# Performance work log

Hardware: AMD Instinct MI355X
Metric: run time of the kernel (lower is better)

The kernel has to match this reference:

```python
import jax, jax.numpy as jnp
import numpy as np

B, L, D, N = 2, 2048, 1024, 16
H = D // N  # head dim 64
MASK_FILL = -100000000.0  # torch code uses -1e8 for non-fp16


def sinusoidal_pos(seq_len, dim):
    # interleaved (sin, cos) table, shape (seq_len, dim); identical per head
    inv_freq = 1.0 / (10000.0 ** (jnp.arange(0, dim, 2, dtype=jnp.float32) / dim))
    ang = jnp.arange(seq_len, dtype=jnp.float32)[:, None] * inv_freq[None, :]
    return jnp.stack([jnp.sin(ang), jnp.cos(ang)], axis=-1).reshape(seq_len, dim)


def apply_rope(x, pos_emb):
    # x: (b, n, l, h); pos_emb: (l, h) interleaved sin/cos
    cos = jnp.repeat(pos_emb[..., 1::2], 2, axis=-1)  # (l, h)
    sin = jnp.repeat(pos_emb[..., ::2], 2, axis=-1)
    x2 = jnp.stack([-x[..., 1::2], x[..., ::2]], axis=-1).reshape(x.shape)
    return x * cos + x2 * sin


def setup_inputs() -> dict:
    key = jax.random.key(0)
    ks = jax.random.split(key, 12)
    inp = {
        "q": jax.random.normal(ks[0], (B, L, D), dtype=jnp.float32),
        "k": jax.random.normal(ks[1], (B, L, D), dtype=jnp.float32),
        "v": jax.random.normal(ks[2], (B, L, D), dtype=jnp.float32),
        "mask": jax.random.bernoulli(ks[3], 0.3, (B, L)),  # True = masked
    }
    s = 0.02
    for i, name in enumerate(["q", "k", "v", "o"]):
        inp[f"W{name}"] = jax.random.normal(ks[4 + i], (D, D), dtype=jnp.float32) * s
        inp[f"b{name}"] = jax.random.normal(ks[8 + i], (D,), dtype=jnp.float32) * s
    return inp


def reference(q, k, v, mask, Wq, bq, Wk, bk, Wv, bv, Wo, bo):
    # projections (torch Linear: x @ W^T + b) and head split -> (b, n, l, h)
    def split_heads(x):
        return x.reshape(B, L, N, H).transpose(0, 2, 1, 3)

    qw = split_heads(q @ Wq.T + bq)
    kw = split_heads(k @ Wk.T + bk)
    vw = split_heads(v @ Wv.T + bv)

    pos = sinusoidal_pos(L, H)
    qw = apply_rope(qw, pos)
    kw = apply_rope(kw, pos)

    # NOTE: original scales by sqrt(hidden_dim), not sqrt(head_dim)
    scores = jnp.einsum("bnlh,bnph->bnlp", qw, kw) / np.sqrt(D).astype(np.float32)
    scores = jnp.where(mask[:, None, None, :], MASK_FILL, scores)
    attn = jax.nn.softmax(scores, axis=-1)  # dropout is identity in eval

    out = jnp.einsum("bnlp,bnph->bnlh", attn, vw)  # (b, n, l, h)
    out = out.transpose(0, 2, 1, 3).reshape(B, L, D)
    return out @ Wo.T + bo
```

## Files before the change

### kernel.cpp

```cpp
#include <hip/hip_runtime.h>
#include <stdint.h>

#define L_SEQ 2048
#define DMODEL 1024
#define NHEAD 16
#define HDIM 64
#define BATCH 2
#define KVBLK 32
#define KHALF (L_SEQ / 2)
#define NKT (KHALF / KVBLK)

typedef __attribute__((ext_vector_type(8))) short bf16x8;
typedef __attribute__((ext_vector_type(4))) float f32x4;

#define MFMA(a, b, c) __builtin_amdgcn_mfma_f32_16x16x32_bf16((a), (b), (c), 0, 0, 0)

#if __has_builtin(__builtin_amdgcn_exp2f)
#define EXP2(x) __builtin_amdgcn_exp2f(x)
#else
#define EXP2(x) exp2f(x)
#endif

#if __has_builtin(__builtin_amdgcn_wave_barrier)
#define WAVE_FENCE() __builtin_amdgcn_wave_barrier()
#else
#define WAVE_FENCE() __syncthreads()
#endif

#define QSCALE 0.04508422f
#define MASKBIAS -100.0f

__device__ __forceinline__ unsigned short f2bf(float f) {
    return (unsigned short)((__float_as_uint(f) + 0x8000u) >> 16);
}
__device__ __forceinline__ float bf2f(unsigned short h) {
    return __uint_as_float(((unsigned int)h) << 16);
}
__device__ __forceinline__ unsigned int pkbf(float a, float b) {
    return __builtin_amdgcn_perm(__float_as_uint(b) + 0x8000u,
                                 __float_as_uint(a) + 0x8000u, 0x07060302u);
}
__device__ __forceinline__ void gl2lds16(const unsigned short* g, unsigned short* l) {
    __builtin_amdgcn_global_load_lds(
        (const __attribute__((address_space(1))) void*)g,
        (__attribute__((address_space(3))) void*)l, 16, 0, 0);
}

__global__ void prep_kernel(
    const float* __restrict__ q, const float* __restrict__ k, const float* __restrict__ v,
    const float* __restrict__ wq, const float* __restrict__ wk, const float* __restrict__ wv,
    const float* __restrict__ Wo, const int* __restrict__ mask,
    unsigned short* __restrict__ xb, unsigned short* __restrict__ wb,
    unsigned short* __restrict__ whi, unsigned short* __restrict__ wlo,
    float2* __restrict__ ropetab, float* __restrict__ fbias)
{
    const int y = blockIdx.y, x = blockIdx.x, tid = threadIdx.x;
    if (y < 6) {
        const float* src = (y == 0) ? q : (y == 1) ? k : (y == 2) ? v
                         : (y == 3) ? wq : (y == 4) ? wk : wv;
        unsigned short* dst = (y < 3) ? xb + (size_t)y * 4194304
                                      : wb + (size_t)(y - 3) * 1048576;
        const int n = (y < 3) ? 4194304 : 1048576;
        const int i = (x * 256 + tid) * 8;
        if (i >= n) return;
        const float4 a = *(const float4*)(src + i);
        const float4 b = *(const float4*)(src + i + 4);
        uint4 u;
        u.x = pkbf(a.x, a.y); u.y = pkbf(a.z, a.w);
        u.z = pkbf(b.x, b.y); u.w = pkbf(b.z, b.w);
        *(uint4*)(dst + i) = u;
    } else if (y == 6) {
        const int i = (x * 256 + tid) * 4;
        if (i >= DMODEL * DMODEL) return;
        const float4 vv = *(const float4*)(Wo + i);
        const float f[4] = {vv.x, vv.y, vv.z, vv.w};
        union { unsigned short s[4]; uint2 u; } h, l;
#pragma unroll
        for (int r = 0; r < 4; ++r) {
            h.s[r] = f2bf(f[r]);
            l.s[r] = f2bf(f[r] - bf2f(h.s[r]));
        }
        *(uint2*)&whi[i] = h.u;
        *(uint2*)&wlo[i] = l.u;
    } else {
        if (x < 512) {
            const int idx = x * 256 + tid;
            const int l = idx >> 6, h = idx & 63;
            const float invf = powf(10000.0f, -(float)(h & 62) * (1.0f / 64.0f));
            float sn, cs;
            sincosf((float)l * invf, &sn, &cs);
            ropetab[idx] = make_float2(cs, sn);
        } else if (x < 528) {
            const int idx = (x - 512) * 256 + tid;
            fbias[idx] = (mask[idx] != 0) ? MASKBIAS : 0.0f;
        }
    }
}

__global__ __launch_bounds__(256) void qkv_kernel(
    const unsigned short* __restrict__ Xb, const unsigned short* __restrict__ Wb,
    const float* __restrict__ bq, const float* __restrict__ bk, const float* __restrict__ bv,
    const float2* __restrict__ ropetab,
    unsigned short* __restrict__ Qd, unsigned short* __restrict__ Kd,
    unsigned short* __restrict__ Vd)
{
    const int id = blockIdx.x;
    const int bx = id / 96, rem = id % 96;
    const int z = rem >> 5, by = rem & 31;

    const unsigned short* X = Xb + (size_t)z * (BATCH * L_SEQ * DMODEL);
    const unsigned short* W = Wb + (size_t)z * (DMODEL * DMODEL);
    const float* bias = (z == 0) ? bq : (z == 1) ? bk : bv;

    __shared__ __align__(16) unsigned short As[128 * 64];
    __shared__ __align__(16) unsigned short Bs[128 * 64];

    const int tid  = threadIdx.x;
    const int wave = tid >> 6, lane = tid & 63;
    const int ml = lane & 15, kq = lane >> 4;
    const int m0 = by * 128, n0 = bx * 128;
    const int wm = (wave & 1) * 64, wn = (wave >> 1) * 64;

    f32x4 acc[4][4];
#pragma unroll
    for (int i = 0; i < 4; ++i)
#pragma unroll
        for (int j = 0; j < 4; ++j) acc[i][j] = (f32x4){0.f, 0.f, 0.f, 0.f};

    const int prow = wave * 32 + (lane >> 3);
    const int pch  = (lane & 7) ^ ((lane >> 3) & 7);
    const unsigned short* gA = X + (size_t)(m0 + prow) * DMODEL + pch * 8;
    const unsigned short* gB = W + (size_t)(n0 + prow) * DMODEL + pch * 8;
    unsigned short* lA = As + wave * 2048;
    unsigned short* lB = Bs + wave * 2048;

    for (int kc = 0; kc < DMODEL; kc += 64) {
#pragma unroll
        for (int qq = 0; qq < 4; ++qq) {
            gl2lds16(gA + kc + (size_t)qq * 8 * DMODEL, lA + qq * 512);
            gl2lds16(gB + kc + (size_t)qq * 8 * DMODEL, lB + qq * 512);
        }
        __syncthreads();

        bf16x8 af[2][4], bfv[2][4];
#pragma unroll
        for (int ks = 0; ks < 2; ++ks)
#pragma unroll
            for (int i = 0; i < 4; ++i) {
                const int Ra = wm + i * 16 + ml;
                af[ks][i] = *(const bf16x8*)&As[Ra * 64 + (((ks * 4 + kq) ^ (Ra & 7)) << 3)];
                const int Rb = wn + i * 16 + ml;
                bfv[ks][i] = *(const bf16x8*)&Bs[Rb * 64 + (((ks * 4 + kq) ^ (Rb & 7)) << 3)];
            }
#pragma unroll
        for (int ks = 0; ks < 2; ++ks)
#pragma unroll
            for (int i = 0; i < 4; ++i)
#pragma unroll
                for (int j = 0; j < 4; ++j)
                    acc[i][j] = MFMA(af[ks][i], bfv[ks][j], acc[i][j]);
        __syncthreads();
    }

    if (z < 2) {
        unsigned short* dst = (z == 0) ? Qd : Kd;
        const float osc = (z == 0) ? QSCALE : 1.0f;
#pragma unroll
        for (int jt = 0; jt < 4; ++jt) {
            const int col = n0 + wn + jt * 16 + ml;
            const float bv = bias[col];
            const int nh = col >> 6, hh = col & 63;
            const int odd = hh & 1;
#pragma unroll
            for (int it = 0; it < 4; ++it) {
#pragma unroll
                for (int r = 0; r < 4; ++r) {
                    const int row = m0 + wm + it * 16 + kq * 4 + r;
                    const int bb = row >> 11, ll = row & 2047;
                    const float v = acc[it][jt][r] + bv;
                    const float partner = __shfl_xor(v, 1);
                    const float2 cs = ropetab[ll * 64 + hh];
                    const float res = odd ? fmaf(v, cs.x, partner * cs.y)
                                          : fmaf(v, cs.x, -partner * cs.y);
                    dst[(((size_t)(bb * NHEAD + nh) * L_SEQ + ll) << 6) + hh] = f2bf(res * osc);
                }
            }
        }
    } else {
#pragma unroll
        for (int jt = 0; jt < 4; ++jt) {
            const int col = n0 + wn + jt * 16 + ml;
            const float bv = bias[col];
            const int nh = col >> 6, hh = col & 63;
#pragma unroll
            for (int it = 0; it < 4; ++it) {
                const int rb = m0 + wm + it * 16 + kq * 4;
                const int bb = rb >> 11, ll = rb & 2047;
                uint2 pk;
                pk.x = pkbf(acc[it][jt][0] + bv, acc[it][jt][1] + bv);
                pk.y = pkbf(acc[it][jt][2] + bv, acc[it][jt][3] + bv);
                *(uint2*)&Vd[(((size_t)bb * NHEAD + nh) * HDIM + hh) * L_SEQ + ll] = pk;
            }
        }
    }
}

__global__ __launch_bounds__(512, 4) void attn_kernel(
    const unsigned short* __restrict__ Qr, const unsigned short* __restrict__ Kr,
    const unsigned short* __restrict__ Vt, const float* __restrict__ fbias,
    unsigned short* __restrict__ AOhi, unsigned short* __restrict__ AOlo)
{
    __shared__ __align__(16) unsigned short lds[24832];

    const int tid  = threadIdx.x;
    const int w    = tid >> 6, lane = tid & 63;
    const int kh   = w >> 2, qg = w & 3;
    const int ml = lane & 15, kq = lane >> 4;

    const int id = blockIdx.x;
    const int xcd = id & 7, slot = id >> 3;
    const int bh = xcd * 4 + (slot & 3);
    const int qb = slot >> 2;
    const int b = bh >> 4, nh = bh & 15;
    const int q0 = qb * 128;
    const int wq = qg * 32;
    const int koff = kh * KHALF;

    const unsigned short* Qp = Qr + (size_t)bh * L_SEQ * HDIM;
    const unsigned short* Kp = Kr + (size_t)bh * L_SEQ * HDIM;
    const unsigned short* Vp = Vt + (size_t)bh * HDIM * L_SEQ;

    bf16x8 qf[2][2];
#pragma unroll
    for (int qt = 0; qt < 2; ++qt)
#pragma unroll
        for (int c = 0; c < 2; ++c)
            qf[qt][c] = *(const bf16x8*)(Qp + (size_t)(q0 + wq + qt * 16 + ml) * HDIM + c * 32 + kq * 8);

    float li[2] = {0.f, 0.f};
    f32x4 o[2][4];
#pragma unroll
    for (int qt = 0; qt < 2; ++qt)
#pragma unroll
        for (int ht = 0; ht < 4; ++ht) o[qt][ht] = (f32x4){0.f, 0.f, 0.f, 0.f};

    unsigned short* Pw = lds + 16384 + w * 1024;

    const int srow8 = lane >> 3;
    const int sch   = (lane & 7) ^ srow8;
    const unsigned short* gK = Kp + (size_t)(koff + qg * 8 + srow8) * HDIM + sch * 8;
    const int vrow = lane >> 2;
    const int vch  = (lane & 3) ^ (vrow & 3);
    const unsigned short* gV = Vp + (size_t)(qg * 16 + vrow) * L_SEQ + koff + vch * 8;

#define STAGE(kt, bf)                                                           \
    do {                                                                        \
        gl2lds16(gK + (size_t)(kt) * KVBLK * HDIM,                              \
                 lds + ((bf) * 2 + kh) * 2048 + qg * 512);                      \
        gl2lds16(gV + (kt) * KVBLK,                                             \
                 lds + 8192 + ((bf) * 2 + kh) * 2048 + qg * 512);               \
    } while (0)

    const float* fbp = fbias + (size_t)b * L_SEQ + koff + kq * 4;
    f32x4 bcur[2], bnext[2];
#pragma unroll
    for (int nt = 0; nt < 2; ++nt) bcur[nt] = *(const f32x4*)(fbp + nt * 16);

    STAGE(0, 0);

    for (int kt = 0; kt < NKT; ++kt) {
        const int buf = kt & 1;
        __syncthreads();
        if (kt + 1 < NKT) {
            STAGE(kt + 1, buf ^ 1);
#pragma unroll
            for (int nt = 0; nt < 2; ++nt)
                bnext[nt] = *(const f32x4*)(fbp + (kt + 1) * KVBLK + nt * 16);
        }

        const unsigned short* Kb = lds + (buf * 2 + kh) * 2048;
        const unsigned short* Vb = lds + 8192 + (buf * 2 + kh) * 2048;

        f32x4 st[2][2];
#pragma unroll
        for (int nt = 0; nt < 2; ++nt) {
            const int R = nt * 16 + ml;
            const bf16x8 kf0 = *(const bf16x8*)&Kb[R * 64 + ((kq ^ (R & 7)) << 3)];
            const bf16x8 kf1 = *(const bf16x8*)&Kb[R * 64 + (((4 + kq) ^ (R & 7)) << 3)];
#pragma unroll
            for (int qt = 0; qt < 2; ++qt) {
                f32x4 c = MFMA(kf0, qf[qt][0], bcur[nt]);
                c = MFMA(kf1, qf[qt][1], c);
                st[qt][nt] = c;
            }
        }

#pragma unroll
        for (int qt = 0; qt < 2; ++qt) {
#pragma unroll
            for (int nt = 0; nt < 2; ++nt) {
                float p[4];
#pragma unroll
                for (int r = 0; r < 4; ++r) {
                    p[r] = EXP2(st[qt][nt][r]);
                    li[qt] += p[r];
                }
                uint2 pk;
                pk.x = pkbf(p[0], p[1]);
                pk.y = pkbf(p[2], p[3]);
                const int row = qt * 16 + ml;
                const int cg = (nt * 2 + (kq >> 1)) ^ (row & 3);
                *(uint2*)&Pw[row * 32 + (cg << 3) + (kq & 1) * 4] = pk;
            }
        }
        WAVE_FENCE();

        bf16x8 pf[2];
#pragma unroll
        for (int qt = 0; qt < 2; ++qt) {
            const int row = qt * 16 + ml;
            pf[qt] = *(const bf16x8*)&Pw[row * 32 + ((kq ^ (row & 3)) << 3)];
        }
#pragma unroll
        for (int ht = 0; ht < 4; ++ht) {
            const int R = ht * 16 + ml;
            const bf16x8 vf = *(const bf16x8*)&Vb[R * 32 + ((kq ^ (R & 3)) << 3)];
#pragma unroll
            for (int qt = 0; qt < 2; ++qt)
                o[qt][ht] = MFMA(vf, pf[qt], o[qt][ht]);
        }
        WAVE_FENCE();

#pragma unroll
        for (int nt = 0; nt < 2; ++nt) bcur[nt] = bnext[nt];
    }
#undef STAGE

#pragma unroll
    for (int qt = 0; qt < 2; ++qt) {
        li[qt] += __shfl_xor(li[qt], 16);
        li[qt] += __shfl_xor(li[qt], 32);
    }

    float* osc = (float*)lds;
    float* lis = (float*)(lds + 24576);
    __syncthreads();
    if (kh == 1) {
#pragma unroll
        for (int qt = 0; qt < 2; ++qt)
#pragma unroll
            for (int ht = 0; ht < 4; ++ht)
                *(f32x4*)(osc + qg * 2048 + (qt * 4 + ht) * 256 + lane * 4) = o[qt][ht];
        if (kq == 0) {
            lis[qg * 32 + ml]      = li[0];
            lis[qg * 32 + 16 + ml] = li[1];
        }
    }
    __syncthreads();
    if (kh == 1) return;

#pragma unroll
    for (int qt = 0; qt < 2; ++qt) {
#pragma unroll
        for (int ht = 0; ht < 4; ++ht)
            o[qt][ht] += *(const f32x4*)(osc + qg * 2048 + (qt * 4 + ht) * 256 + lane * 4);
        li[qt] += lis[qg * 32 + qt * 16 + ml];
    }
    const float inv[2] = {1.f / li[0], 1.f / li[1]};

    unsigned short* Pe = lds + 16384 + qg * 2048;
    const int qr = lane >> 2, quarter = lane & 3;
    const int rc0 = (quarter * 2) ^ (qr & 7), rc1 = (quarter * 2 + 1) ^ (qr & 7);

#pragma unroll
    for (int qt = 0; qt < 2; ++qt)
#pragma unroll
        for (int ht = 0; ht < 4; ++ht) {
            uint2 pk;
            pk.x = pkbf(o[qt][ht][0] * inv[qt], o[qt][ht][1] * inv[qt]);
            pk.y = pkbf(o[qt][ht][2] * inv[qt], o[qt][ht][3] * inv[qt]);
            const int row = qt * 16 + ml;
            const int ck = ht * 2 + (kq >> 1);
            *(uint2*)&Pe[row * 64 + ((ck ^ (ml & 7)) << 3) + (kq & 1) * 4] = pk;
        }
    WAVE_FENCE();
#pragma unroll
    for (int qt = 0; qt < 2; ++qt) {
        const size_t gbase = ((size_t)b * L_SEQ + q0 + wq + qt * 16 + qr) * DMODEL
                             + nh * 64 + quarter * 16;
        const uint4 d0 = *(const uint4*)&Pe[(qt * 16 + qr) * 64 + (rc0 << 3)];
        const uint4 d1 = *(const uint4*)&Pe[(qt * 16 + qr) * 64 + (rc1 << 3)];
        *(uint4*)&AOhi[gbase]     = d0;
        *(uint4*)&AOhi[gbase + 8] = d1;
    }
    WAVE_FENCE();
#pragma unroll
    for (int qt = 0; qt < 2; ++qt)
#pragma unroll
        for (int ht = 0; ht < 4; ++ht) {
            float lo[4];
#pragma unroll
            for (int r = 0; r < 4; ++r) {
                const float v = o[qt][ht][r] * inv[qt];
                const float hf = __uint_as_float((__float_as_uint(v) + 0x8000u) & 0xffff0000u);
                lo[r] = v - hf;
            }
            uint2 pk;
            pk.x = pkbf(lo[0], lo[1]);
            pk.y = pkbf(lo[2], lo[3]);
            const int row = qt * 16 + ml;
            const int ck = ht * 2 + (kq >> 1);
            *(uint2*)&Pe[row * 64 + ((ck ^ (ml & 7)) << 3) + (kq & 1) * 4] = pk;
        }
    WAVE_FENCE();
#pragma unroll
    for (int qt = 0; qt < 2; ++qt) {
        const size_t gbase = ((size_t)b * L_SEQ + q0 + wq + qt * 16 + qr) * DMODEL
                             + nh * 64 + quarter * 16;
        const uint4 d0 = *(const uint4*)&Pe[(qt * 16 + qr) * 64 + (rc0 << 3)];
        const uint4 d1 = *(const uint4*)&Pe[(qt * 16 + qr) * 64 + (rc1 << 3)];
        *(uint4*)&AOlo[gbase]     = d0;
        *(uint4*)&AOlo[gbase + 8] = d1;
    }
}

__global__ __launch_bounds__(256) void oproj_kernel(
    const unsigned short* __restrict__ Ahi_g, const unsigned short* __restrict__ Alo_g,
    const unsigned short* __restrict__ Whi_g, const unsigned short* __restrict__ Wlo_g,
    const float* __restrict__ bias, float* __restrict__ out)
{
    const int id = blockIdx.x;
    const int bxn = id >> 5, by = id & 31;

    __shared__ __align__(16) unsigned short Ah[128 * 32], Al[128 * 32];
    __shared__ __align__(16) unsigned short Bh[64 * 32],  Bl[64 * 32];

    const int tid  = threadIdx.x;
    const int wave = tid >> 6, lane = tid & 63;
    const int ml = lane & 15, kq = lane >> 4;
    const int m0 = by * 128, n0 = bxn * 64;
    const int wm = (wave & 1) * 64, wn = (wave >> 1) * 32;

    f32x4 acc[4][2];
#pragma unroll
    for (int i = 0; i < 4; ++i)
#pragma unroll
        for (int j = 0; j < 2; ++j) acc[i][j] = (f32x4){0.f, 0.f, 0.f, 0.f};

    const int rl  = lane >> 2;
    const int pch = (lane & 3) ^ ((lane >> 3) & 3);
    const int prowA = wave * 32 + rl;
    const int prowB = wave * 16 + rl;
    const unsigned short* gAh = Ahi_g + (size_t)(m0 + prowA) * DMODEL + pch * 8;
    const unsigned short* gAl = Alo_g + (size_t)(m0 + prowA) * DMODEL + pch * 8;
    const unsigned short* gBh = Whi_g + (size_t)(n0 + prowB) * DMODEL + pch * 8;
    const unsigned short* gBl = Wlo_g + (size_t)(n0 + prowB) * DMODEL + pch * 8;
    unsigned short* lAh = Ah + wave * 1024;
    unsigned short* lAl = Al + wave * 1024;
    unsigned short* lBh = Bh + wave * 512;
    unsigned short* lBl = Bl + wave * 512;

    for (int kc = 0; kc < DMODEL; kc += 32) {
#pragma unroll
        for (int qq = 0; qq < 2; ++qq) {
            const size_t go = kc + (size_t)qq * 16 * DMODEL;
            gl2lds16(gAh + go, lAh + qq * 512);
            gl2lds16(gAl + go, lAl + qq * 512);
        }
        gl2lds16(gBh + kc, lBh);
        gl2lds16(gBl + kc, lBl);
        __syncthreads();

        bf16x8 ah[4], al[4], bh_[2], bl_[2];
#pragma unroll
        for (int i = 0; i < 4; ++i) {
            const int Ra = wm + i * 16 + ml;
            const int sa = Ra * 32 + ((kq ^ ((Ra >> 1) & 3)) << 3);
            ah[i] = *(const bf16x8*)&Ah[sa];
            al[i] = *(const bf16x8*)&Al[sa];
        }
#pragma unroll
        for (int j = 0; j < 2; ++j) {
            const int Rb = wn + j * 16 + ml;
            const int sb = Rb * 32 + ((kq ^ ((Rb >> 1) & 3)) << 3);
            bh_[j] = *(const bf16x8*)&Bh[sb];
            bl_[j] = *(const bf16x8*)&Bl[sb];
        }
#pragma unroll
        for (int i = 0; i < 4; ++i)
#pragma unroll
            for (int j = 0; j < 2; ++j) {
                acc[i][j] = MFMA(ah[i], bh_[j], acc[i][j]);
                acc[i][j] = MFMA(al[i], bh_[j], acc[i][j]);
                acc[i][j] = MFMA(ah[i], bl_[j], acc[i][j]);
            }
        __syncthreads();
    }

#pragma unroll
    for (int jt = 0; jt < 2; ++jt) {
        const int col = n0 + wn + jt * 16 + ml;
        const float bv = bias[col];
#pragma unroll
        for (int it = 0; it < 4; ++it)
#pragma unroll
            for (int r = 0; r < 4; ++r) {
                const int row = m0 + wm + it * 16 + kq * 4 + r;
                out[(size_t)row * DMODEL + col] = acc[it][jt][r] + bv;
            }
    }
}

extern "C" void kernel_launch(void* const* d_in, const int* in_sizes, int n_in,
                              void* d_out, int out_size, void* d_ws, size_t ws_size,
                              hipStream_t stream)
{
    (void)in_sizes; (void)n_in; (void)out_size; (void)ws_size;
    const float* q    = (const float*)d_in[0];
    const float* k    = (const float*)d_in[1];
    const float* v    = (const float*)d_in[2];
    const int*   mask = (const int*)d_in[3];
    const float* Wq   = (const float*)d_in[4];
    const float* bq   = (const float*)d_in[5];
    const float* Wk   = (const float*)d_in[6];
    const float* bk   = (const float*)d_in[7];
    const float* Wv   = (const float*)d_in[8];
    const float* bv   = (const float*)d_in[9];
    const float* Wo   = (const float*)d_in[10];
    const float* bo   = (const float*)d_in[11];
    float* out = (float*)d_out;

    const size_t HE = (size_t)BATCH * NHEAD * L_SEQ * HDIM;
    const size_t DD = (size_t)DMODEL * DMODEL;
    unsigned short* Xb   = (unsigned short*)d_ws;
    unsigned short* Wb   = Xb + 3 * HE;
    unsigned short* Qr   = Wb + 3 * DD;
    unsigned short* Kr   = Qr + HE;
    unsigned short* Vt   = Kr + HE;
    unsigned short* Whi  = Vt + HE;
    unsigned short* Wlo  = Whi + DD;
    float* fbias = (float*)(Wlo + DD);
    float2* ropetab = (float2*)(fbias + (size_t)BATCH * L_SEQ);
    unsigned short* AOhi = Xb;
    unsigned short* AOlo = Xb + HE;

    prep_kernel<<<dim3(2048, 8), dim3(256), 0, stream>>>(
        q, k, v, Wq, Wk, Wv, Wo, mask, Xb, Wb, Whi, Wlo, ropetab, fbias);

    qkv_kernel<<<dim3(768), dim3(256), 0, stream>>>(Xb, Wb, bq, bk, bv, ropetab, Qr, Kr, Vt);

    attn_kernel<<<dim3(512), dim3(512), 0, stream>>>(Qr, Kr, Vt, fbias, AOhi, AOlo);

    oproj_kernel<<<dim3(512), dim3(256), 0, stream>>>(AOhi, AOlo, Whi, Wlo, bo, out);
}
```

Baseline: 246.5 us.

## Halve attention block to 4 waves, each handling 64 query rows

The attention kernel now runs 256 threads (4 waves) instead of 512. Each wave processes 64 query rows instead of 32, so every K/V fragment read from LDS feeds twice as many MFMAs, and staging, swizzle and epilogue offsets are adjusted to match. This cuts LDS traffic and barrier participants per unit of work, but raises register pressure (larger o/st/qf arrays) and halves per-block parallelism, which may lower occupancy or latency hiding.

```diff
diff --git a/kernel.cpp b/kernel.cpp
--- a/kernel.cpp
+++ b/kernel.cpp
@@ -205,7 +205,7 @@
     }
 }
 
-__global__ __launch_bounds__(512, 4) void attn_kernel(
+__global__ __launch_bounds__(256) void attn_kernel(
     const unsigned short* __restrict__ Qr, const unsigned short* __restrict__ Kr,
     const unsigned short* __restrict__ Vt, const float* __restrict__ fbias,
     unsigned short* __restrict__ AOhi, unsigned short* __restrict__ AOlo)
@@ -214,8 +214,9 @@
 
     const int tid  = threadIdx.x;
     const int w    = tid >> 6, lane = tid & 63;
-    const int kh   = w >> 2, qg = w & 3;
+    const int kh   = w >> 1, qg = w & 1;
     const int ml = lane & 15, kq = lane >> 4;
+    const int swz = (ml >> 1) & 3;
 
     const int id = blockIdx.x;
     const int xcd = id & 7, slot = id >> 3;
@@ -223,42 +224,44 @@
     const int qb = slot >> 2;
     const int b = bh >> 4, nh = bh & 15;
     const int q0 = qb * 128;
-    const int wq = qg * 32;
+    const int wq = qg * 64;
     const int koff = kh * KHALF;
 
     const unsigned short* Qp = Qr + (size_t)bh * L_SEQ * HDIM;
     const unsigned short* Kp = Kr + (size_t)bh * L_SEQ * HDIM;
     const unsigned short* Vp = Vt + (size_t)bh * HDIM * L_SEQ;
 
-    bf16x8 qf[2][2];
-#pragma unroll
-    for (int qt = 0; qt < 2; ++qt)
+    bf16x8 qf[4][2];
+#pragma unroll
+    for (int qt = 0; qt < 4; ++qt)
 #pragma unroll
         for (int c = 0; c < 2; ++c)
             qf[qt][c] = *(const bf16x8*)(Qp + (size_t)(q0 + wq + qt * 16 + ml) * HDIM + c * 32 + kq * 8);
 
-    float li[2] = {0.f, 0.f};
-    f32x4 o[2][4];
-#pragma unroll
-    for (int qt = 0; qt < 2; ++qt)
+    float li[4] = {0.f, 0.f, 0.f, 0.f};
+    f32x4 o[4][4];
+#pragma unroll
+    for (int qt = 0; qt < 4; ++qt)
 #pragma unroll
         for (int ht = 0; ht < 4; ++ht) o[qt][ht] = (f32x4){0.f, 0.f, 0.f, 0.f};
 
-    unsigned short* Pw = lds + 16384 + w * 1024;
+    unsigned short* Pw = lds + 16384 + w * 2048;
 
     const int srow8 = lane >> 3;
     const int sch   = (lane & 7) ^ srow8;
-    const unsigned short* gK = Kp + (size_t)(koff + qg * 8 + srow8) * HDIM + sch * 8;
+    const unsigned short* gK = Kp + (size_t)(koff + qg * 16 + srow8) * HDIM + sch * 8;
     const int vrow = lane >> 2;
-    const int vch  = (lane & 3) ^ (vrow & 3);
-    const unsigned short* gV = Vp + (size_t)(qg * 16 + vrow) * L_SEQ + koff + vch * 8;
+    const int vch  = (lane & 3) ^ ((vrow >> 1) & 3);
+    const unsigned short* gV = Vp + (size_t)(qg * 32 + vrow) * L_SEQ + koff + vch * 8;
 
 #define STAGE(kt, bf)                                                           \
     do {                                                                        \
-        gl2lds16(gK + (size_t)(kt) * KVBLK * HDIM,                              \
-                 lds + ((bf) * 2 + kh) * 2048 + qg * 512);                      \
-        gl2lds16(gV + (kt) * KVBLK,                                             \
-                 lds + 8192 + ((bf) * 2 + kh) * 2048 + qg * 512);               \
+        unsigned short* kb = lds + ((bf) * 2 + kh) * 2048 + qg * 1024;          \
+        unsigned short* vb = lds + 8192 + ((bf) * 2 + kh) * 2048 + qg * 1024;   \
+        gl2lds16(gK + (size_t)(kt) * KVBLK * HDIM, kb);                         \
+        gl2lds16(gK + (size_t)((kt) * KVBLK + 8) * HDIM, kb + 512);             \
+        gl2lds16(gV + (kt) * KVBLK, vb);                                        \
+        gl2lds16(gV + (size_t)16 * L_SEQ + (kt) * KVBLK, vb + 512);             \
     } while (0)
 
     const float* fbp = fbias + (size_t)b * L_SEQ + koff + kq * 4;
@@ -281,14 +284,14 @@
         const unsigned short* Kb = lds + (buf * 2 + kh) * 2048;
         const unsigned short* Vb = lds + 8192 + (buf * 2 + kh) * 2048;
 
-        f32x4 st[2][2];
+        f32x4 st[4][2];
 #pragma unroll
         for (int nt = 0; nt < 2; ++nt) {
             const int R = nt * 16 + ml;
             const bf16x8 kf0 = *(const bf16x8*)&Kb[R * 64 + ((kq ^ (R & 7)) << 3)];
             const bf16x8 kf1 = *(const bf16x8*)&Kb[R * 64 + (((4 + kq) ^ (R & 7)) << 3)];
 #pragma unroll
-            for (int qt = 0; qt < 2; ++qt) {
+            for (int qt = 0; qt < 4; ++qt) {
                 f32x4 c = MFMA(kf0, qf[qt][0], bcur[nt]);
                 c = MFMA(kf1, qf[qt][1], c);
                 st[qt][nt] = c;
@@ -296,7 +299,7 @@
         }
 
 #pragma unroll
-        for (int qt = 0; qt < 2; ++qt) {
+        for (int qt = 0; qt < 4; ++qt) {
 #pragma unroll
             for (int nt = 0; nt < 2; ++nt) {
                 float p[4];
@@ -309,24 +312,24 @@
                 pk.x = pkbf(p[0], p[1]);
                 pk.y = pkbf(p[2], p[3]);
                 const int row = qt * 16 + ml;
-                const int cg = (nt * 2 + (kq >> 1)) ^ (row & 3);
+                const int cg = (nt * 2 + (kq >> 1)) ^ swz;
                 *(uint2*)&Pw[row * 32 + (cg << 3) + (kq & 1) * 4] = pk;
             }
         }
         WAVE_FENCE();
 
-        bf16x8 pf[2];
-#pragma unroll
-        for (int qt = 0; qt < 2; ++qt) {
+        bf16x8 pf[4];
+#pragma unroll
+        for (int qt = 0; qt < 4; ++qt) {
             const int row = qt * 16 + ml;
-            pf[qt] = *(const bf16x8*)&Pw[row * 32 + ((kq ^ (row & 3)) << 3)];
+            pf[qt] = *(const bf16x8*)&Pw[row * 32 + ((kq ^ swz) << 3)];
         }
 #pragma unroll
         for (int ht = 0; ht < 4; ++ht) {
             const int R = ht * 16 + ml;
-            const bf16x8 vf = *(const bf16x8*)&Vb[R * 32 + ((kq ^ (R & 3)) << 3)];
-#pragma unroll
-            for (int qt = 0; qt < 2; ++qt)
+            const bf16x8 vf = *(const bf16x8*)&Vb[R * 32 + ((kq ^ swz) << 3)];
+#pragma unroll
+            for (int qt = 0; qt < 4; ++qt)
                 o[qt][ht] = MFMA(vf, pf[qt], o[qt][ht]);
         }
         WAVE_FENCE();
@@ -337,7 +340,7 @@
 #undef STAGE
 
 #pragma unroll
-    for (int qt = 0; qt < 2; ++qt) {
+    for (int qt = 0; qt < 4; ++qt) {
         li[qt] += __shfl_xor(li[qt], 16);
         li[qt] += __shfl_xor(li[qt], 32);
     }
@@ -347,33 +350,35 @@
     __syncthreads();
     if (kh == 1) {
 #pragma unroll
-        for (int qt = 0; qt < 2; ++qt)
+        for (int qt = 0; qt < 4; ++qt)
 #pragma unroll
             for (int ht = 0; ht < 4; ++ht)
-                *(f32x4*)(osc + qg * 2048 + (qt * 4 + ht) * 256 + lane * 4) = o[qt][ht];
+                *(f32x4*)(osc + qg * 4096 + (qt * 4 + ht) * 256 + lane * 4) = o[qt][ht];
         if (kq == 0) {
-            lis[qg * 32 + ml]      = li[0];
-            lis[qg * 32 + 16 + ml] = li[1];
+#pragma unroll
+            for (int qt = 0; qt < 4; ++qt)
+                lis[qg * 64 + qt * 16 + ml] = li[qt];
         }
     }
     __syncthreads();
     if (kh == 1) return;
 
-#pragma unroll
-    for (int qt = 0; qt < 2; ++qt) {
+    float inv[4];
+#pragma unroll
+    for (int qt = 0; qt < 4; ++qt) {
 #pragma unroll
         for (int ht = 0; ht < 4; ++ht)
-            o[qt][ht] += *(const f32x4*)(osc + qg * 2048 + (qt * 4 + ht) * 256 + lane * 4);
-        li[qt] += lis[qg * 32 + qt * 16 + ml];
-    }
-    const float inv[2] = {1.f / li[0], 1.f / li[1]};
-
-    unsigned short* Pe = lds + 16384 + qg * 2048;
+            o[qt][ht] += *(const f32x4*)(osc + qg * 4096 + (qt * 4 + ht) * 256 + lane * 4);
+        li[qt] += lis[qg * 64 + qt * 16 + ml];
+        inv[qt] = 1.f / li[qt];
+    }
+
+    unsigned short* Pe = lds + 16384 + qg * 4096;
     const int qr = lane >> 2, quarter = lane & 3;
     const int rc0 = (quarter * 2) ^ (qr & 7), rc1 = (quarter * 2 + 1) ^ (qr & 7);
 
 #pragma unroll
-    for (int qt = 0; qt < 2; ++qt)
+    for (int qt = 0; qt < 4; ++qt)
 #pragma unroll
         for (int ht = 0; ht < 4; ++ht) {
             uint2 pk;
@@ -385,7 +390,7 @@
         }
     WAVE_FENCE();
 #pragma unroll
-    for (int qt = 0; qt < 2; ++qt) {
+    for (int qt = 0; qt < 4; ++qt) {
         const size_t gbase = ((size_t)b * L_SEQ + q0 + wq + qt * 16 + qr) * DMODEL
                              + nh * 64 + quarter * 16;
         const uint4 d0 = *(const uint4*)&Pe[(qt * 16 + qr) * 64 + (rc0 << 3)];
@@ -395,7 +400,7 @@
     }
     WAVE_FENCE();
 #pragma unroll
-    for (int qt = 0; qt < 2; ++qt)
+    for (int qt = 0; qt < 4; ++qt)
 #pragma unroll
         for (int ht = 0; ht < 4; ++ht) {
             float lo[4];
@@ -414,7 +419,7 @@
         }
     WAVE_FENCE();
 #pragma unroll
-    for (int qt = 0; qt < 2; ++qt) {
+    for (int qt = 0; qt < 4; ++qt) {
         const size_t gbase = ((size_t)b * L_SEQ + q0 + wq + qt * 16 + qr) * DMODEL
                              + nh * 64 + quarter * 16;
         const uint4 d0 = *(const uint4*)&Pe[(qt * 16 + qr) * 64 + (rc0 << 3)];
@@ -549,7 +554,7 @@
 
     qkv_kernel<<<dim3(768), dim3(256), 0, stream>>>(Xb, Wb, bq, bk, bv, ropetab, Qr, Kr, Vt);
 
-    attn_kernel<<<dim3(512), dim3(512), 0, stream>>>(Qr, Kr, Vt, fbias, AOhi, AOlo);
+    attn_kernel<<<dim3(512), dim3(256), 0, stream>>>(Qr, Kr, Vt, fbias, AOhi, AOlo);
 
     oproj_kernel<<<dim3(512), dim3(256), 0, stream>>>(AOhi, AOlo, Whi, Wlo, bo, out);
 }
```

Measured after the change: 264.4 us. 7.2% more time.
